# Kernel optimization log

Measured on AMD Instinct MI355X. Metric: run time of the kernel, lower is better.

The kernel has to match this reference:

```python
import jax, jax.numpy as jnp
import numpy as np

N_NODES = 50000
N_EDGES = 1600000


def setup_inputs() -> dict:
    key = jax.random.key(0)
    ks = jax.random.split(key, 8)
    dims = [1024, 2048, 1024, 512]
    fea = jax.random.normal(ks[0], (N_NODES, dims[0]), dtype=jnp.float32)
    edge_index = jax.random.randint(ks[1], (2, N_EDGES), 0, N_NODES, dtype=jnp.int64)
    edge_vals = jax.random.uniform(ks[2], (N_EDGES,), dtype=jnp.float32)
    # Glorot-ish scaled weights per GCN layer
    W1 = jax.random.normal(ks[3], (dims[0], dims[1]), dtype=jnp.float32) / np.sqrt(dims[0])
    W2 = jax.random.normal(ks[4], (dims[1], dims[2]), dtype=jnp.float32) / np.sqrt(dims[1])
    W3 = jax.random.normal(ks[5], (dims[2], dims[3]), dtype=jnp.float32) / np.sqrt(dims[2])
    b1 = jnp.zeros((dims[1],), dtype=jnp.float32)
    b2 = jnp.zeros((dims[2],), dtype=jnp.float32)
    b3 = jnp.zeros((dims[3],), dtype=jnp.float32)
    return {"fea": fea, "edge_index": edge_index, "edge_vals": edge_vals,
            "W1": W1, "b1": b1, "W2": W2, "b2": b2, "W3": W3, "b3": b3}


def _gcn_layer(x, row, col, edge_vals, W, b):
    # dense transform: [N, din] @ [din, dout] + bias
    support = x @ W + b
    # spmm(adj, support) in COO form: out[row] += val * support[col]
    msgs = support[col] * edge_vals[:, None]          # [E, dout]
    return jax.ops.segment_sum(msgs, row, num_segments=N_NODES)


def reference(fea, edge_index, edge_vals, W1, b1, W2, b2, W3, b3):
    row, col = edge_index[0], edge_index[1]
    h = jax.nn.relu(_gcn_layer(fea, row, col, edge_vals, W1, b1))
    h = jax.nn.relu(_gcn_layer(h, row, col, edge_vals, W2, b2))
    # last layer: no activation
    return _gcn_layer(h, row, col, edge_vals, W3, b3)
```

## Files before the change

kernel.cpp:

```cpp
#include <hip/hip_runtime.h>

typedef unsigned short u16;
using bf16x8 = __attribute__((ext_vector_type(8))) short;
using u16x8  = __attribute__((ext_vector_type(8))) unsigned short;
using u16x4  = __attribute__((ext_vector_type(4))) unsigned short;
using f32x4  = __attribute__((ext_vector_type(4))) float;

#define NN 50000
#define NPAD 50176

__device__ __forceinline__ u16 f2b(float f) {
  union { float f; unsigned u; } x; x.f = f;
  unsigned r = x.u + 0x7fffu + ((x.u >> 16) & 1u);
  return (u16)(r >> 16);
}
__device__ __forceinline__ float b2f(u16 h) {
  union { unsigned u; float f; } x; x.u = ((unsigned)h) << 16; return x.f;
}

#define GLOAD_LDS16(g, l) __builtin_amdgcn_global_load_lds( \
    (const __attribute__((address_space(1))) unsigned int*)(g), \
    (__attribute__((address_space(3))) unsigned int*)(l), 16, 0, 0)

__global__ void hist_kernel(const int* __restrict__ rows, const float* __restrict__ vals,
                            int* __restrict__ counts, float* __restrict__ rowsum, int E) {
  int e = blockIdx.x * 256 + threadIdx.x;
  if (e < E) {
    int r = rows[e];
    atomicAdd(&counts[r], 1);
    atomicAdd(&rowsum[r], vals[e]);
  }
}

__global__ void scan_bsum(const int* __restrict__ counts, int* __restrict__ bsum, int n) {
  __shared__ int s[256];
  int t = threadIdx.x;
  int gi = blockIdx.x * 256 + t;
  s[t] = (gi < n) ? counts[gi] : 0;
  __syncthreads();
  for (int d = 128; d > 0; d >>= 1) {
    if (t < d) s[t] += s[t + d];
    __syncthreads();
  }
  if (t == 0) bsum[blockIdx.x] = s[0];
}

__global__ void scan_partials(int* __restrict__ bsum, int nb) {
  __shared__ int s[256];
  int t = threadIdx.x;
  int v = (t < nb) ? bsum[t] : 0;
  s[t] = v;
  __syncthreads();
  for (int d = 1; d < 256; d <<= 1) {
    int x = (t >= d) ? s[t - d] : 0;
    __syncthreads();
    s[t] += x;
    __syncthreads();
  }
  if (t < nb) bsum[t] = s[t] - v;
}

__global__ void scan_final(const int* __restrict__ counts, const int* __restrict__ bsum,
                           int* __restrict__ offs, int n) {
  __shared__ int s[256];
  int t = threadIdx.x;
  int gi = blockIdx.x * 256 + t;
  int v = (gi < n) ? counts[gi] : 0;
  s[t] = v;
  __syncthreads();
  for (int d = 1; d < 256; d <<= 1) {
    int x = (t >= d) ? s[t - d] : 0;
    __syncthreads();
    s[t] += x;
    __syncthreads();
  }
  if (gi <= n) offs[gi] = bsum[blockIdx.x] + s[t] - v;
}

__global__ void scatter_kernel(const int* __restrict__ rows, const int* __restrict__ cols,
                               const float* __restrict__ vals, const int* __restrict__ offs,
                               int* __restrict__ cursor, int* __restrict__ ecol,
                               float* __restrict__ ev2, int E) {
  int e = blockIdx.x * 256 + threadIdx.x;
  if (e < E) {
    int r = rows[e];
    int p = offs[r] + atomicAdd(&cursor[r], 1);
    ecol[p] = cols[e];
    ev2[p] = vals[e];
  }
}

__global__ void conv_f2b4(const float* __restrict__ in, u16* __restrict__ out, int n4) {
  int i = blockIdx.x * 256 + threadIdx.x;
  if (i < n4) {
    float4 f = ((const float4*)in)[i];
    ushort4 o;
    o.x = f2b(f.x); o.y = f2b(f.y); o.z = f2b(f.z); o.w = f2b(f.w);
    ((ushort4*)out)[i] = o;
  }
}

__global__ void transpose_conv(const float* __restrict__ W, u16* __restrict__ Wt, int K, int N) {
  __shared__ float tile[32][33];
  int bx = blockIdx.x * 32;
  int by = blockIdx.y * 32;
  int tx = threadIdx.x;
  int ty = threadIdx.y;
  for (int i = 0; i < 32; i += 8) tile[ty + i][tx] = W[(size_t)(by + ty + i) * N + bx + tx];
  __syncthreads();
  for (int i = 0; i < 32; i += 8) Wt[(size_t)(bx + ty + i) * K + by + tx] = f2b(tile[tx][ty + i]);
}

__global__ __launch_bounds__(512, 4)
void gemm256(const u16* __restrict__ A, const u16* __restrict__ Bt,
             const float* __restrict__ bias, const float* __restrict__ rowsum,
             u16* __restrict__ C, int M, int N, int K, int relu, int nbx) {
  __shared__ __align__(16) u16 As[2][256 * 32];
  __shared__ __align__(16) u16 Bs[2][128 * 32];

  const int p = blockIdx.x, total = gridDim.x;
  const int q = total >> 3, r8 = total & 7;
  const int xcd = p & 7, slot_ = p >> 3;
  const int l = (xcd < r8 ? xcd * (q + 1) : r8 * (q + 1) + (xcd - r8) * q) + slot_;
  const int bm = (l / nbx) * 256;
  const int bn = (l % nbx) * 128;

  const int tid = threadIdx.x;
  const int lane = tid & 63;
  const int wid = tid >> 6;
  const int wm = wid >> 1;
  const int wn = wid & 1;
  const int l15 = lane & 15, lg = lane >> 4;

  const int trow = tid >> 2;
  const int xcol = (tid & 3) ^ ((tid >> 3) & 3);
  const u16* gA = A + (size_t)(bm + trow) * K + xcol * 8;
  const u16* gB = Bt + (size_t)(bn + trow) * K + xcol * 8;
  const size_t rowstep = (size_t)128 * K;

  f32x4 acc[4][4];
#pragma unroll
  for (int i = 0; i < 4; i++)
#pragma unroll
    for (int j = 0; j < 4; j++)
#pragma unroll
      for (int k = 0; k < 4; k++) acc[i][j][k] = 0.f;

  const int NT = K >> 5;

#define STAGE(kt, b)                                                           \
  {                                                                            \
    const u16* sa = gA + (size_t)(kt) * 32;                                    \
    u16* da = &As[b][0] + tid * 8;                                             \
    GLOAD_LDS16(sa, da);                                                       \
    GLOAD_LDS16(sa + rowstep, da + 4096);                                      \
    const u16* sb = gB + (size_t)(kt) * 32;                                    \
    GLOAD_LDS16(sb, &Bs[b][0] + tid * 8);                                      \
  }

  STAGE(0, 0);

  for (int u = 0; u < NT; u++) {
    const int cb = u & 1;
    if (u + 1 < NT) {
      STAGE(u + 1, cb ^ 1);
      asm volatile("s_waitcnt vmcnt(3)" ::: "memory");
    } else {
      asm volatile("s_waitcnt vmcnt(0)" ::: "memory");
    }
    __builtin_amdgcn_s_barrier();

    const u16* ab = &As[cb][0];
    const u16* bb = &Bs[cb][0];

    bf16x8 bfr[4];
#pragma unroll
    for (int n = 0; n < 4; n++) {
      int row = wn * 64 + n * 16 + l15;
      int s = lg ^ ((row >> 1) & 3);
      bfr[n] = *(const bf16x8*)&bb[row * 32 + s * 8];
    }
    __builtin_amdgcn_s_setprio(1);
#pragma unroll
    for (int m = 0; m < 4; m++) {
      int row = wm * 64 + m * 16 + l15;
      int s = lg ^ ((row >> 1) & 3);
      bf16x8 am = *(const bf16x8*)&ab[row * 32 + s * 8];
#pragma unroll
      for (int n = 0; n < 4; n++)
        acc[m][n] = __builtin_amdgcn_mfma_f32_16x16x32_bf16(am, bfr[n], acc[m][n], 0, 0, 0);
    }
    __builtin_amdgcn_s_setprio(0);
    asm volatile("s_waitcnt lgkmcnt(0)" ::: "memory");
    __builtin_amdgcn_s_barrier();
  }
#undef STAGE

  float bs[4];
#pragma unroll
  for (int n = 0; n < 4; n++) bs[n] = bias[bn + wn * 64 + n * 16 + l15];
#pragma unroll
  for (int m = 0; m < 4; m++) {
    int rowb = bm + wm * 64 + m * 16 + lg * 4;
#pragma unroll
    for (int j = 0; j < 4; j++) {
      int row = rowb + j;
      if (row < M) {
        float rs = rowsum ? rowsum[row] : 1.0f;
#pragma unroll
        for (int n = 0; n < 4; n++) {
          int col = bn + wn * 64 + n * 16 + l15;
          float v = acc[m][n][j] + rs * bs[n];
          if (relu) v = fmaxf(v, 0.f);
          C[(size_t)row * N + col] = f2b(v);
        }
      }
    }
  }
}

template <int VEC, int RELU, int OUTF32>
__global__ __launch_bounds__(64)
void spmm3(const int* __restrict__ offs, const int* __restrict__ ecol,
           const float* __restrict__ ev, const u16* __restrict__ X,
           void* __restrict__ outp, int stride) {
  const int node = blockIdx.x;
  const int t = threadIdx.x;
  const int s0 = offs[node];
  const int e0 = offs[node + 1];
  float acc[VEC];
#pragma unroll
  for (int k = 0; k < VEC; k++) acc[k] = 0.f;
  const u16* __restrict__ Xc = X + (size_t)t * VEC;

  int j = s0;
  for (; j + 4 <= e0; j += 4) {
    const int c0 = ecol[j], c1 = ecol[j + 1], c2 = ecol[j + 2], c3 = ecol[j + 3];
    const float v0 = ev[j], v1 = ev[j + 1], v2 = ev[j + 2], v3 = ev[j + 3];
    u16 a0[VEC], a1[VEC], a2[VEC], a3[VEC];
    if constexpr (VEC == 8) {
      *(u16x8*)a0 = *(const u16x8*)(Xc + (size_t)c0 * stride);
      *(u16x8*)a1 = *(const u16x8*)(Xc + (size_t)c1 * stride);
      *(u16x8*)a2 = *(const u16x8*)(Xc + (size_t)c2 * stride);
      *(u16x8*)a3 = *(const u16x8*)(Xc + (size_t)c3 * stride);
    } else {
      *(u16x4*)a0 = *(const u16x4*)(Xc + (size_t)c0 * stride);
      *(u16x4*)a1 = *(const u16x4*)(Xc + (size_t)c1 * stride);
      *(u16x4*)a2 = *(const u16x4*)(Xc + (size_t)c2 * stride);
      *(u16x4*)a3 = *(const u16x4*)(Xc + (size_t)c3 * stride);
    }
#pragma unroll
    for (int k = 0; k < VEC; k++) acc[k] += v0 * b2f(a0[k]);
#pragma unroll
    for (int k = 0; k < VEC; k++) acc[k] += v1 * b2f(a1[k]);
#pragma unroll
    for (int k = 0; k < VEC; k++) acc[k] += v2 * b2f(a2[k]);
#pragma unroll
    for (int k = 0; k < VEC; k++) acc[k] += v3 * b2f(a3[k]);
  }
  for (; j < e0; j++) {
    const int c0 = ecol[j];
    const float v0 = ev[j];
    u16 a0[VEC];
    if constexpr (VEC == 8) {
      *(u16x8*)a0 = *(const u16x8*)(Xc + (size_t)c0 * stride);
    } else {
      *(u16x4*)a0 = *(const u16x4*)(Xc + (size_t)c0 * stride);
    }
#pragma unroll
    for (int k = 0; k < VEC; k++) acc[k] += v0 * b2f(a0[k]);
  }

  if (RELU) {
#pragma unroll
    for (int k = 0; k < VEC; k++) acc[k] = fmaxf(acc[k], 0.f);
  }
  if (OUTF32) {
    float* o = (float*)outp + (size_t)node * stride + (size_t)t * VEC;
#pragma unroll
    for (int k = 0; k < VEC; k += 4) {
      f32x4 st;
      st[0] = acc[k]; st[1] = acc[k + 1]; st[2] = acc[k + 2]; st[3] = acc[k + 3];
      __builtin_nontemporal_store(st, (f32x4*)(o + k));
    }
  } else {
    u16* o = (u16*)outp + (size_t)node * stride + (size_t)t * VEC;
    if constexpr (VEC == 8) {
      u16x8 st;
#pragma unroll
      for (int k = 0; k < 8; k++) st[k] = f2b(acc[k]);
      __builtin_nontemporal_store(st, (u16x8*)o);
    } else {
      u16x4 st;
      st[0] = f2b(acc[0]); st[1] = f2b(acc[1]); st[2] = f2b(acc[2]); st[3] = f2b(acc[3]);
      __builtin_nontemporal_store(st, (u16x4*)o);
    }
  }
}

extern "C" void kernel_launch(void* const* d_in, const int* in_sizes, int n_in,
                              void* d_out, int out_size, void* d_ws, size_t ws_size,
                              hipStream_t stream) {
  const float* fea = (const float*)d_in[0];
  const int* ei = (const int*)d_in[1];
  const float* ev = (const float*)d_in[2];
  const float* W1 = (const float*)d_in[3];
  const float* b1 = (const float*)d_in[4];
  const float* W2 = (const float*)d_in[5];
  const float* b2 = (const float*)d_in[6];
  const float* W3 = (const float*)d_in[7];
  const float* b3 = (const float*)d_in[8];
  const int E = in_sizes[1] / 2;
  const int* erow = ei;
  const int* ecol_in = ei + E;

  char* w = (char*)d_ws;
  auto alloc = [&](size_t bytes) {
    char* p = w;
    w += (bytes + 255) & ~(size_t)255;
    return p;
  };
  u16* fea_b = (u16*)alloc((size_t)NPAD * 1024 * 2);
  u16* bufB  = (u16*)alloc((size_t)NPAD * 1024 * 2);
  u16* h1_b  = (u16*)alloc((size_t)NPAD * 2048 * 2);
  u16* t2_b  = (u16*)alloc((size_t)NPAD * 1024 * 2);
  u16* W1t = (u16*)alloc((size_t)2048 * 1024 * 2);
  u16* W2t = (u16*)alloc((size_t)1024 * 2048 * 2);
  u16* W3t = (u16*)alloc((size_t)512 * 1024 * 2);
  float* rowsum = (float*)alloc((size_t)NN * 4);
  int* counts = (int*)alloc((size_t)NN * 4);
  int* cursor = (int*)alloc((size_t)NN * 4);
  int* offs = (int*)alloc((size_t)(NN + 1) * 4);
  int* ecol = (int*)alloc((size_t)E * 4);
  float* ev2 = (float*)alloc((size_t)E * 4);
  int* bsum = (int*)alloc(256 * 4);
  (void)bsum; (void)ws_size; (void)n_in; (void)out_size;

  hipMemsetAsync(rowsum, 0, (size_t)((char*)offs - (char*)rowsum), stream);

  const int eb = (E + 255) / 256;
  const int nb = (NN + 256) / 256;
  hist_kernel<<<eb, 256, 0, stream>>>(erow, ev, counts, rowsum, E);
  scan_bsum<<<nb, 256, 0, stream>>>(counts, bsum, NN);
  scan_partials<<<1, 256, 0, stream>>>(bsum, nb);
  scan_final<<<nb, 256, 0, stream>>>(counts, bsum, offs, NN);
  scatter_kernel<<<eb, 256, 0, stream>>>(erow, ecol_in, ev, offs, cursor, ecol, ev2, E);

  conv_f2b4<<<(NN * 1024 / 4 + 255) / 256, 256, 0, stream>>>(fea, fea_b, NN * 1024 / 4);
  dim3 tb(32, 8);
  transpose_conv<<<dim3(2048 / 32, 1024 / 32), tb, 0, stream>>>(W1, W1t, 1024, 2048);
  transpose_conv<<<dim3(1024 / 32, 2048 / 32), tb, 0, stream>>>(W2, W2t, 2048, 1024);
  transpose_conv<<<dim3(512 / 32, 1024 / 32), tb, 0, stream>>>(W3, W3t, 1024, 512);

  const int MT2 = (NN + 255) / 256;
  spmm3<8, 0, 0><<<NN, 64, 0, stream>>>(offs, ecol, ev2, fea_b, bufB, 1024);
  spmm3<8, 0, 0><<<NN, 64, 0, stream>>>(offs, ecol, ev2, fea_b + 512, bufB + 512, 1024);
  gemm256<<<(2048 / 128) * MT2, 512, 0, stream>>>(bufB, W1t, b1, rowsum, h1_b, NN, 2048, 1024, 1, 2048 / 128);
  gemm256<<<(1024 / 128) * MT2, 512, 0, stream>>>(h1_b, W2t, b2, nullptr, t2_b, NN, 1024, 2048, 0, 1024 / 128);
  spmm3<8, 1, 0><<<NN, 64, 0, stream>>>(offs, ecol, ev2, t2_b, fea_b, 1024);
  spmm3<8, 1, 0><<<NN, 64, 0, stream>>>(offs, ecol, ev2, t2_b + 512, fea_b + 512, 1024);
  gemm256<<<(512 / 128) * MT2, 512, 0, stream>>>(fea_b, W3t, b3, nullptr, bufB, NN, 512, 1024, 0, 512 / 128);
  spmm3<4, 0, 1><<<NN, 64, 0, stream>>>(offs, ecol, ev2, bufB, d_out, 512);
  spmm3<4, 0, 1><<<NN, 64, 0, stream>>>(offs, ecol, ev2, bufB + 256, (float*)d_out + 256, 512);
}
```

Baseline: 2.077 ms.

## Triple-buffer GEMM K-loop and stage epilogue through LDS for coalesced stores

The bf16 GEMM now uses a three-stage LDS ring, prefetching two K-tiles ahead with matching vmcnt waits, so global-to-LDS loads have more time to overlap the MFMA work. The epilogue writes results into a swizzled per-wave LDS tile and then stores 16-byte rows to C, replacing scattered 2-byte global stores. The cost is LDS per block rising from 48KB to 72KB, which can lower the number of resident blocks per CU. The epilogue also reads rowsum for padded rows beyond M before bounds checking.

New measurement: 1.995 ms, median of 2. -3.9%, faster.

```diff
diff --git a/kernel.cpp b/kernel.cpp
--- a/kernel.cpp
+++ b/kernel.cpp
@@ -115,8 +115,7 @@
 void gemm256(const u16* __restrict__ A, const u16* __restrict__ Bt,
              const float* __restrict__ bias, const float* __restrict__ rowsum,
              u16* __restrict__ C, int M, int N, int K, int relu, int nbx) {
-  __shared__ __align__(16) u16 As[2][256 * 32];
-  __shared__ __align__(16) u16 Bs[2][128 * 32];
+  __shared__ __align__(16) u16 lds[3][12288];
 
   const int p = blockIdx.x, total = gridDim.x;
   const int q = total >> 3, r8 = total & 7;
@@ -151,27 +150,30 @@
 #define STAGE(kt, b)                                                           \
   {                                                                            \
     const u16* sa = gA + (size_t)(kt) * 32;                                    \
-    u16* da = &As[b][0] + tid * 8;                                             \
+    u16* da = &lds[b][0] + tid * 8;                                            \
     GLOAD_LDS16(sa, da);                                                       \
     GLOAD_LDS16(sa + rowstep, da + 4096);                                      \
     const u16* sb = gB + (size_t)(kt) * 32;                                    \
-    GLOAD_LDS16(sb, &Bs[b][0] + tid * 8);                                      \
+    GLOAD_LDS16(sb, &lds[b][8192] + tid * 8);                                  \
   }
 
   STAGE(0, 0);
+  STAGE(1, 1);
 
   for (int u = 0; u < NT; u++) {
-    const int cb = u & 1;
-    if (u + 1 < NT) {
-      STAGE(u + 1, cb ^ 1);
+    const int cb = u % 3;
+    if (u + 2 < NT) {
+      STAGE(u + 2, (u + 2) % 3);
+      asm volatile("s_waitcnt vmcnt(6)" ::: "memory");
+    } else if (u + 1 < NT) {
       asm volatile("s_waitcnt vmcnt(3)" ::: "memory");
     } else {
       asm volatile("s_waitcnt vmcnt(0)" ::: "memory");
     }
     __builtin_amdgcn_s_barrier();
 
-    const u16* ab = &As[cb][0];
-    const u16* bb = &Bs[cb][0];
+    const u16* ab = &lds[cb][0];
+    const u16* bb = &lds[cb][8192];
 
     bf16x8 bfr[4];
 #pragma unroll
@@ -196,26 +198,37 @@
   }
 #undef STAGE
 
+  u16* eb = &lds[0][0] + wid * 4096;
   float bs[4];
 #pragma unroll
   for (int n = 0; n < 4; n++) bs[n] = bias[bn + wn * 64 + n * 16 + l15];
 #pragma unroll
   for (int m = 0; m < 4; m++) {
-    int rowb = bm + wm * 64 + m * 16 + lg * 4;
+    int r0 = m * 16 + lg * 4;
 #pragma unroll
     for (int j = 0; j < 4; j++) {
-      int row = rowb + j;
-      if (row < M) {
-        float rs = rowsum ? rowsum[row] : 1.0f;
-#pragma unroll
-        for (int n = 0; n < 4; n++) {
-          int col = bn + wn * 64 + n * 16 + l15;
-          float v = acc[m][n][j] + rs * bs[n];
-          if (relu) v = fmaxf(v, 0.f);
-          C[(size_t)row * N + col] = f2b(v);
-        }
+      int r = r0 + j;
+      float rs = rowsum ? rowsum[bm + wm * 64 + r] : 1.0f;
+#pragma unroll
+      for (int n = 0; n < 4; n++) {
+        int c = n * 16 + l15;
+        float v = acc[m][n][j] + rs * bs[n];
+        if (relu) v = fmaxf(v, 0.f);
+        int cs = (c & 7) | ((((c >> 3) ^ (r & 7)) & 7) << 3);
+        eb[r * 64 + cs] = f2b(v);
       }
     }
+  }
+  asm volatile("s_waitcnt lgkmcnt(0)" ::: "memory");
+#pragma unroll
+  for (int pass = 0; pass < 8; pass++) {
+    int r = pass * 8 + (lane >> 3);
+    int ch = lane & 7;
+    int chs = ch ^ (r & 7);
+    u16x8 val = *(const u16x8*)&eb[r * 64 + chs * 8];
+    int grow = bm + wm * 64 + r;
+    if (grow < M)
+      *(u16x8*)&C[(size_t)grow * N + bn + wn * 64 + ch * 8] = val;
   }
 }
 
```
